# Performance work log

Measured on AMD Instinct MI355X. Metric: run time of the kernel, lower is better.

## Reference

```python
import jax, jax.numpy as jnp
import numpy as np

K = 3  # kernel height/width (filter_size = (1, 3, 3), nF = 9)


def _extract_patches(x):
    """x: [B, C, H, W] -> patches [B, C, H, W, K*K], matching the identity
    grouped conv2d (cross-correlation) with padding=1 in the original:
    patch index i = dy*K + dx corresponds to x[c, h+dy-1, w+dx-1]."""
    B, C, H, W = x.shape
    xp = jnp.pad(x, ((0, 0), (0, 0), (1, 1), (1, 1)))
    # fixed K*K=9 offsets: small static loop, not a data-dim loop
    return jnp.stack(
        [xp[:, :, dy:dy + H, dx:dx + W] for dy in range(K) for dx in range(K)],
        axis=-1,
    )


def setup_inputs() -> dict:
    key = jax.random.key(0)
    k1, k2 = jax.random.split(key)
    B, C, H, W = 4, 128, 180, 320
    nF = K * K
    x = jax.random.normal(k1, (B, C, H, W), dtype=jnp.float32)
    filters = jax.random.normal(k2, (B, nF, H, W), dtype=jnp.float32)
    return {"x": x, "filters": filters}


def reference(x, filters):
    """x: [B, 128, H, W]; filters: [B, 9, H, W]. Returns [B, 128, H, W].
    Equivalent to: im2col (identity grouped conv) then per-pixel matmul
    [128, 9] @ [9, 1] at every spatial location."""
    patches = _extract_patches(x)                       # [B, C, H, W, 9]
    f = jnp.transpose(filters, (0, 2, 3, 1))            # [B, H, W, 9]
    out = jnp.einsum('bchwf,bhwf->bchw', patches, f)    # per-pixel dot
    return out
```

## Files before the change

### kernel.cpp

```cpp
#include <hip/hip_runtime.h>


#define CC 128
#define HH 180
#define W4 80
#define WW (W4 * 4)
#define NF 9
#define CPT 8
#define H2 (HH / 2)
#define NCG (CC / CPT)

__device__ __forceinline__ void fma_row(float4& acc, const float4 f0, const float4 f1,
                                        const float4 f2, const float aL, const float4 B,
                                        const float cR) {
    acc.x = fmaf(f0.x, aL,  fmaf(f1.x, B.x, fmaf(f2.x, B.y, acc.x)));
    acc.y = fmaf(f0.y, B.x, fmaf(f1.y, B.y, fmaf(f2.y, B.z, acc.y)));
    acc.z = fmaf(f0.z, B.y, fmaf(f1.z, B.z, fmaf(f2.z, B.w, acc.z)));
    acc.w = fmaf(f0.w, B.z, fmaf(f1.w, B.w, fmaf(f2.w, cR,  acc.w)));
}

__global__ __launch_bounds__(256, 4) void duf_kernel(
    const float* __restrict__ x,
    const float* __restrict__ f,
    float* __restrict__ out)
{
    int n = blockIdx.x * 256 + threadIdx.x;
    int w4 = n % W4;
    int t  = n / W4;
    int cg = t % NCG;
    t /= NCG;
    int h2 = t % H2;
    int b  = t / H2;
    int h  = h2 * 2;

    const float4* f4 = (const float4*)f;
    float4* o4 = (float4*)out;

    float4 fr0[NF], fr1[NF];
    size_t fbase = ((size_t)(b * NF) * HH + h) * W4 + w4;
#pragma unroll
    for (int i = 0; i < NF; ++i) {
        fr0[i] = f4[fbase + (size_t)i * HH * W4];
        fr1[i] = f4[fbase + (size_t)i * HH * W4 + W4];
    }

    const bool at_l = (w4 == 0);
    const bool at_r = (w4 == W4 - 1);

    const int c0 = cg * CPT;
    for (int cc = 0; cc < CPT; ++cc) {
        const float* xc = x + (size_t)(b * CC + c0 + cc) * HH * WW;
        float4 a0 = make_float4(0.f, 0.f, 0.f, 0.f);
        float4 a1 = make_float4(0.f, 0.f, 0.f, 0.f);
#pragma unroll
        for (int r = 0; r < 4; ++r) {
            int hr = h - 1 + r;
            float4 B = make_float4(0.f, 0.f, 0.f, 0.f);
            float aL = 0.f, cR = 0.f;
            if (hr >= 0 && hr < HH) {
                const float* xr = xc + (size_t)hr * WW;
                B = *(const float4*)(xr + w4 * 4);
                if (!at_l) aL = xr[w4 * 4 - 1];
                if (!at_r) cR = xr[w4 * 4 + 4];
            }
            if (r < 3) fma_row(a0, fr0[3*r  ], fr0[3*r+1], fr0[3*r+2], aL, B, cR);
            if (r > 0) fma_row(a1, fr1[3*r-3], fr1[3*r-2], fr1[3*r-1], aL, B, cR);
        }
        size_t ob = ((size_t)(b * CC + c0 + cc) * HH + h) * W4 + w4;
        o4[ob]      = a0;
        o4[ob + W4] = a1;
    }
}

extern "C" void kernel_launch(void* const* d_in, const int* in_sizes, int n_in,
                              void* d_out, int out_size, void* d_ws, size_t ws_size,
                              hipStream_t stream) {
    const float* x = (const float*)d_in[0];
    const float* f = (const float*)d_in[1];
    float* out = (float*)d_out;

    int B = in_sizes[0] / (CC * HH * W4 * 4 * 4);
    (void)B;
    int total = 4 * H2 * NCG * W4;
    duf_kernel<<<total / 256, 256, 0, stream>>>(x, f, out);
}
```

Baseline: 239.6 us.

## Stage filters in shared memory, one channel per thread, XCD-aware block swizzle

Each block now covers a 16-channel by 16-float4 width tile of two output rows. The 9 filter rows for that tile are staged once into shared memory instead of each thread holding 18 float4 filter registers across an 8-channel loop. Block indices are remapped so consecutive tiles land on the same XCD, so the 8 channel groups sharing a filter tile hit the same L2. This lowers register pressure and raises parallelism, at the cost of a barrier, LDS reads and redundant filter loads per channel group.

```diff
diff --git a/kernel.cpp b/kernel.cpp
--- a/kernel.cpp
+++ b/kernel.cpp
@@ -4,11 +4,16 @@
 #define CC 128
 #define HH 180
 #define W4 80
-#define WW (W4 * 4)
 #define NF 9
-#define CPT 8
-#define H2 (HH / 2)
-#define NCG (CC / CPT)
+#define H2 90
+#define CLPB 16
+#define WLPB 16
+#define WS 5
+#define CGRPS (CC / CLPB)
+#define NXCD 8
+#define TILES (4 * H2 * WS)
+#define TPX (TILES / NXCD)
+#define NBLK (TILES * CGRPS)
 
 __device__ __forceinline__ void fma_row(float4& acc, const float4 f0, const float4 f1,
                                         const float4 f2, const float aL, const float4 B,
@@ -19,57 +24,72 @@
     acc.w = fmaf(f0.w, B.z, fmaf(f1.w, B.w, fmaf(f2.w, cR,  acc.w)));
 }
 
-__global__ __launch_bounds__(256, 4) void duf_kernel(
+__global__ __launch_bounds__(256) void duf_kernel(
     const float* __restrict__ x,
     const float* __restrict__ f,
     float* __restrict__ out)
 {
-    int n = blockIdx.x * 256 + threadIdx.x;
-    int w4 = n % W4;
-    int t  = n / W4;
-    int cg = t % NCG;
-    t /= NCG;
-    int h2 = t % H2;
-    int b  = t / H2;
-    int h  = h2 * 2;
+    int raw = blockIdx.x;
+    int xcd = raw & 7;
+    int li  = raw >> 3;
+    int cgrp = li & 7;
+    int tl   = li >> 3;
+    int tile = xcd * TPX + tl;
+    int b   = tile / (H2 * WS);
+    int rem = tile % (H2 * WS);
+    int h2  = rem / WS;
+    int ws  = rem % WS;
+    int h   = h2 * 2;
+
+    int tid = threadIdx.x;
+    int wl  = tid & 15;
+    int cl  = tid >> 4;
+    int c   = cgrp * CLPB + cl;
+    int gw4 = ws * WLPB + wl;
 
     const float4* f4 = (const float4*)f;
     float4* o4 = (float4*)out;
 
-    float4 fr0[NF], fr1[NF];
-    size_t fbase = ((size_t)(b * NF) * HH + h) * W4 + w4;
+    __shared__ float4 fl[NF * 2 * WLPB];
+    for (int s = tid; s < NF * 2 * WLPB; s += 256) {
+        int swl = s & 15;
+        int sr  = (s >> 4) & 1;
+        int si  = s >> 5;
+        fl[s] = f4[((size_t)(b * NF + si) * HH + h + sr) * W4 + ws * WLPB + swl];
+    }
+    __syncthreads();
+
+    const size_t xcbase = (size_t)(b * CC + c) * HH * W4;
+    float4 a0 = make_float4(0.f, 0.f, 0.f, 0.f);
+    float4 a1 = make_float4(0.f, 0.f, 0.f, 0.f);
 #pragma unroll
-    for (int i = 0; i < NF; ++i) {
-        fr0[i] = f4[fbase + (size_t)i * HH * W4];
-        fr1[i] = f4[fbase + (size_t)i * HH * W4 + W4];
+    for (int r = 0; r < 4; ++r) {
+        int hr = h - 1 + r;
+        float4 B = make_float4(0.f, 0.f, 0.f, 0.f);
+        float aL = 0.f, cR = 0.f;
+        if (hr >= 0 && hr < HH) {
+            const float* xr = x + (xcbase + (size_t)hr * W4) * 4;
+            B = *(const float4*)(xr + gw4 * 4);
+            if (gw4 > 0)      aL = xr[gw4 * 4 - 1];
+            if (gw4 < W4 - 1) cR = xr[gw4 * 4 + 4];
+        }
+        if (r < 3) {
+            float4 f0 = fl[((3 * r + 0) * 2 + 0) * 16 + wl];
+            float4 f1 = fl[((3 * r + 1) * 2 + 0) * 16 + wl];
+            float4 f2 = fl[((3 * r + 2) * 2 + 0) * 16 + wl];
+            fma_row(a0, f0, f1, f2, aL, B, cR);
+        }
+        if (r > 0) {
+            float4 g0 = fl[((3 * r - 3) * 2 + 1) * 16 + wl];
+            float4 g1 = fl[((3 * r - 2) * 2 + 1) * 16 + wl];
+            float4 g2 = fl[((3 * r - 1) * 2 + 1) * 16 + wl];
+            fma_row(a1, g0, g1, g2, aL, B, cR);
+        }
     }
 
-    const bool at_l = (w4 == 0);
-    const bool at_r = (w4 == W4 - 1);
-
-    const int c0 = cg * CPT;
-    for (int cc = 0; cc < CPT; ++cc) {
-        const float* xc = x + (size_t)(b * CC + c0 + cc) * HH * WW;
-        float4 a0 = make_float4(0.f, 0.f, 0.f, 0.f);
-        float4 a1 = make_float4(0.f, 0.f, 0.f, 0.f);
-#pragma unroll
-        for (int r = 0; r < 4; ++r) {
-            int hr = h - 1 + r;
-            float4 B = make_float4(0.f, 0.f, 0.f, 0.f);
-            float aL = 0.f, cR = 0.f;
-            if (hr >= 0 && hr < HH) {
-                const float* xr = xc + (size_t)hr * WW;
-                B = *(const float4*)(xr + w4 * 4);
-                if (!at_l) aL = xr[w4 * 4 - 1];
-                if (!at_r) cR = xr[w4 * 4 + 4];
-            }
-            if (r < 3) fma_row(a0, fr0[3*r  ], fr0[3*r+1], fr0[3*r+2], aL, B, cR);
-            if (r > 0) fma_row(a1, fr1[3*r-3], fr1[3*r-2], fr1[3*r-1], aL, B, cR);
-        }
-        size_t ob = ((size_t)(b * CC + c0 + cc) * HH + h) * W4 + w4;
-        o4[ob]      = a0;
-        o4[ob + W4] = a1;
-    }
+    size_t ob = ((size_t)(b * CC + c) * HH + h) * W4 + gw4;
+    o4[ob]      = a0;
+    o4[ob + W4] = a1;
 }
 
 extern "C" void kernel_launch(void* const* d_in, const int* in_sizes, int n_in,
@@ -78,9 +98,5 @@
     const float* x = (const float*)d_in[0];
     const float* f = (const float*)d_in[1];
     float* out = (float*)d_out;
-
-    int B = in_sizes[0] / (CC * HH * W4 * 4 * 4);
-    (void)B;
-    int total = 4 * H2 * NCG * W4;
-    duf_kernel<<<total / 256, 256, 0, stream>>>(x, f, out);
+    duf_kernel<<<NBLK, 256, 0, stream>>>(x, f, out);
 }
```

After: 250.4 us. 1.04x slower.

## Process one row per thread with double-buffered channel prefetch and XCD-aware block remap

Applied to the files above, without the earlier changes.

Each thread now produces one output row instead of two, dropping the 4-row sliding window. The next channel's input rows are prefetched into registers while the current one is computed. Edge handling moves from per-load branches to clamped addresses plus zeroed filter taps. Block indices are remapped so that contiguous block ranges land on the same XCD. In exchange, vertical reuse of input rows within a thread is lost: each input row is now loaded three times instead of twice per two outputs, so more L2 traffic is expected.

```diff
diff --git a/kernel.cpp b/kernel.cpp
--- a/kernel.cpp
+++ b/kernel.cpp
@@ -3,72 +3,90 @@
 
 #define CC 128
 #define HH 180
+#define WW 320
 #define W4 80
-#define WW (W4 * 4)
 #define NF 9
 #define CPT 8
-#define H2 (HH / 2)
-#define NCG (CC / CPT)
-
-__device__ __forceinline__ void fma_row(float4& acc, const float4 f0, const float4 f1,
-                                        const float4 f2, const float aL, const float4 B,
-                                        const float cR) {
-    acc.x = fmaf(f0.x, aL,  fmaf(f1.x, B.x, fmaf(f2.x, B.y, acc.x)));
-    acc.y = fmaf(f0.y, B.x, fmaf(f1.y, B.y, fmaf(f2.y, B.z, acc.y)));
-    acc.z = fmaf(f0.z, B.y, fmaf(f1.z, B.z, fmaf(f2.z, B.w, acc.z)));
-    acc.w = fmaf(f0.w, B.z, fmaf(f1.w, B.w, fmaf(f2.w, cR,  acc.w)));
-}
+#define CQ  (CC / CPT)
+#define CST (HH * WW)
+#define NTHR (4 * HH * CQ * W4)
+#define NBLK (NTHR / 256)
+#define XCHUNK (NBLK / 8)
 
 __global__ __launch_bounds__(256, 4) void duf_kernel(
     const float* __restrict__ x,
     const float* __restrict__ f,
     float* __restrict__ out)
 {
-    int n = blockIdx.x * 256 + threadIdx.x;
+    int raw = blockIdx.x;
+    int wg  = (raw & 7) * XCHUNK + (raw >> 3);
+    int n   = wg * 256 + threadIdx.x;
+
     int w4 = n % W4;
     int t  = n / W4;
-    int cg = t % NCG;
-    t /= NCG;
-    int h2 = t % H2;
-    int b  = t / H2;
-    int h  = h2 * 2;
+    int cq = t % CQ;
+    t /= CQ;
+    int h  = t % HH;
+    int b  = t / HH;
 
     const float4* f4 = (const float4*)f;
     float4* o4 = (float4*)out;
+    const float4 z4 = make_float4(0.f, 0.f, 0.f, 0.f);
 
-    float4 fr0[NF], fr1[NF];
-    size_t fbase = ((size_t)(b * NF) * HH + h) * W4 + w4;
+    float4 fw[NF];
+    size_t fb = ((size_t)(b * NF) * HH + h) * W4 + w4;
 #pragma unroll
-    for (int i = 0; i < NF; ++i) {
-        fr0[i] = f4[fbase + (size_t)i * HH * W4];
-        fr1[i] = f4[fbase + (size_t)i * HH * W4 + W4];
+    for (int i = 0; i < NF; ++i) fw[i] = f4[fb + (size_t)i * (HH * W4)];
+    if (h == 0)      { fw[0] = z4; fw[1] = z4; fw[2] = z4; }
+    if (h == HH - 1) { fw[6] = z4; fw[7] = z4; fw[8] = z4; }
+    if (w4 == 0)     { fw[0].x = 0.f; fw[3].x = 0.f; fw[6].x = 0.f; }
+    if (w4 == W4-1)  { fw[2].w = 0.f; fw[5].w = 0.f; fw[8].w = 0.f; }
+
+    const int wB = w4 * 4;
+    const int wA = (w4 == 0)      ? wB     : wB - 1;
+    const int wC = (w4 == W4 - 1) ? wB + 3 : wB + 4;
+    const int r0 = (h == 0)       ? 0      : h - 1;
+    const int r2 = (h == HH - 1)  ? HH - 1 : h + 1;
+    unsigned orow[3] = { (unsigned)(r0 * WW), (unsigned)(h * WW), (unsigned)(r2 * WW) };
+    const unsigned cbase = (unsigned)(b * CC + cq * CPT) * (unsigned)CST;
+
+    float4 Bv[2][3]; float aLv[2][3], cRv[2][3];
+
+#pragma unroll
+    for (int r = 0; r < 3; ++r) {
+        const float* p = x + (size_t)(cbase + orow[r]);
+        Bv[0][r]  = *(const float4*)(p + wB);
+        aLv[0][r] = p[wA];
+        cRv[0][r] = p[wC];
     }
 
-    const bool at_l = (w4 == 0);
-    const bool at_r = (w4 == W4 - 1);
+    size_t ob = ((size_t)(b * CC + cq * CPT) * HH + h) * W4 + w4;
 
-    const int c0 = cg * CPT;
-    for (int cc = 0; cc < CPT; ++cc) {
-        const float* xc = x + (size_t)(b * CC + c0 + cc) * HH * WW;
-        float4 a0 = make_float4(0.f, 0.f, 0.f, 0.f);
-        float4 a1 = make_float4(0.f, 0.f, 0.f, 0.f);
 #pragma unroll
-        for (int r = 0; r < 4; ++r) {
-            int hr = h - 1 + r;
-            float4 B = make_float4(0.f, 0.f, 0.f, 0.f);
-            float aL = 0.f, cR = 0.f;
-            if (hr >= 0 && hr < HH) {
-                const float* xr = xc + (size_t)hr * WW;
-                B = *(const float4*)(xr + w4 * 4);
-                if (!at_l) aL = xr[w4 * 4 - 1];
-                if (!at_r) cR = xr[w4 * 4 + 4];
+    for (int k = 0; k < CPT; ++k) {
+        const int cur = k & 1, nxt = cur ^ 1;
+        if (k + 1 < CPT) {
+            const unsigned cb = cbase + (unsigned)((k + 1) * CST);
+#pragma unroll
+            for (int r = 0; r < 3; ++r) {
+                const float* p = x + (size_t)(cb + orow[r]);
+                Bv[nxt][r]  = *(const float4*)(p + wB);
+                aLv[nxt][r] = p[wA];
+                cRv[nxt][r] = p[wC];
             }
-            if (r < 3) fma_row(a0, fr0[3*r  ], fr0[3*r+1], fr0[3*r+2], aL, B, cR);
-            if (r > 0) fma_row(a1, fr1[3*r-3], fr1[3*r-2], fr1[3*r-1], aL, B, cR);
         }
-        size_t ob = ((size_t)(b * CC + c0 + cc) * HH + h) * W4 + w4;
-        o4[ob]      = a0;
-        o4[ob + W4] = a1;
+        float4 acc = z4;
+#pragma unroll
+        for (int r = 0; r < 3; ++r) {
+            const float4 f0 = fw[3*r], f1 = fw[3*r+1], f2 = fw[3*r+2];
+            const float4 B = Bv[cur][r];
+            const float aL = aLv[cur][r], cR = cRv[cur][r];
+            acc.x = fmaf(f0.x, aL,  fmaf(f1.x, B.x, fmaf(f2.x, B.y, acc.x)));
+            acc.y = fmaf(f0.y, B.x, fmaf(f1.y, B.y, fmaf(f2.y, B.z, acc.y)));
+            acc.z = fmaf(f0.z, B.y, fmaf(f1.z, B.z, fmaf(f2.z, B.w, acc.z)));
+            acc.w = fmaf(f0.w, B.z, fmaf(f1.w, B.w, fmaf(f2.w, cR,  acc.w)));
+        }
+        o4[ob + (size_t)k * (HH * W4)] = acc;
     }
 }
 
@@ -78,9 +96,5 @@
     const float* x = (const float*)d_in[0];
     const float* f = (const float*)d_in[1];
     float* out = (float*)d_out;
-
-    int B = in_sizes[0] / (CC * HH * W4 * 4 * 4);
-    (void)B;
-    int total = 4 * H2 * NCG * W4;
-    duf_kernel<<<total / 256, 256, 0, stream>>>(x, f, out);
+    duf_kernel<<<NBLK, 256, 0, stream>>>(x, f, out);
 }
```

New measurement: 256.9 us. +7.2%, slower.
